# Kernel tuning notes

Measured on AMD Instinct MI355X. Metric: run time of the kernel, lower is better.

## Reference

```python
import jax, jax.numpy as jnp
import numpy as np

N = 50000          # total nodes
E = 800000         # edges (avg degree 16)
IN = 128           # in_feat
HID = 64           # hidden per head
HEADS = (4, 4, 1)
NEG_SLOPE = 0.2    # DGL GATConv leaky_relu default


def setup_inputs() -> dict:
    key = jax.random.key(0)
    ks = jax.random.split(key, 16)

    def w(k, shape, fan_in):
        return jax.random.normal(k, shape, jnp.float32) / np.float32(np.sqrt(fan_in))

    inp = {
        "feat": jax.random.normal(ks[0], (N, IN), jnp.float32),
        "src": jax.random.randint(ks[1], (E,), 0, N, jnp.int32),
        "dst": jax.random.randint(ks[2], (E,), 0, N, jnp.int32),
    }
    dims = [(IN, HEADS[0]), (HID * HEADS[0], HEADS[1]), (HID * HEADS[1], HEADS[2])]
    j = 3
    for i, (din, h) in enumerate(dims, 1):
        inp[f"W{i}"] = w(ks[j], (din, h * HID), din); j += 1
        inp[f"al{i}"] = w(ks[j], (h, HID), HID); j += 1
        inp[f"ar{i}"] = w(ks[j], (h, HID), HID); j += 1
        inp[f"b{i}"] = jnp.zeros((h * HID,), jnp.float32)
    return inp


def gat_layer(x, W, al, ar, b, src, dst, n_heads):
    # DGL GATConv: linear -> per-node attn logits -> edge leaky_relu ->
    # per-dst segment softmax -> weighted scatter-sum -> + bias
    h = (x @ W).reshape(N, n_heads, HID)                     # [N,H,D]
    el = jnp.einsum("nhd,hd->nh", h, al)                     # [N,H]
    er = jnp.einsum("nhd,hd->nh", h, ar)                     # [N,H]
    e = jax.nn.leaky_relu(el[src] + er[dst], NEG_SLOPE)      # [E,H]
    m = jax.ops.segment_max(e, dst, num_segments=N)          # [N,H]
    m = jnp.where(jnp.isfinite(m), m, 0.0)                   # empty segments -> -inf
    ex = jnp.exp(e - m[dst])                                 # [E,H]
    s = jax.ops.segment_sum(ex, dst, num_segments=N)         # [N,H]
    alpha = ex / s[dst]                                      # [E,H]
    msg = h[src] * alpha[:, :, None]                         # [E,H,D]
    out = jax.ops.segment_sum(msg, dst, num_segments=N)      # [N,H,D]
    return out + b.reshape(1, n_heads, HID)


def reference(feat, src, dst, W1, al1, ar1, b1, W2, al2, ar2, b2, W3, al3, ar3, b3):
    h = jax.nn.elu(gat_layer(feat, W1, al1, ar1, b1, src, dst, HEADS[0]))
    h = h.reshape(N, HEADS[0] * HID)                         # flatten heads
    h = jax.nn.elu(gat_layer(h, W2, al2, ar2, b2, src, dst, HEADS[1]))
    h = h.reshape(N, HEADS[1] * HID)
    h = gat_layer(h, W3, al3, ar3, b3, src, dst, HEADS[2])   # no activation
    return h.mean(axis=1)                                    # [N, HID]
```

## Files before the change

kernel.cpp:

```cpp
#include <hip/hip_runtime.h>
#include <math.h>

#define HID 64
#define NSLOPE 0.2f
#define SB 512

typedef __attribute__((ext_vector_type(8))) short short8v;
typedef __attribute__((ext_vector_type(4))) float float4v;

__device__ inline unsigned short f2bf(float x) {
  unsigned u = __float_as_uint(x);
  u += 0x7fffu + ((u >> 16) & 1u);
  return (unsigned short)(u >> 16);
}
__device__ inline float bf2f(unsigned short h) {
  return __uint_as_float(((unsigned)h) << 16);
}
__device__ inline float bflo(unsigned u) { return __uint_as_float(u << 16); }
__device__ inline float bfhi(unsigned u) { return __uint_as_float(u & 0xffff0000u); }

__global__ __launch_bounds__(256) void k_split(const float* __restrict__ x,
    unsigned short* __restrict__ hi, unsigned short* __restrict__ lo, int n) {
  int i = blockIdx.x * 256 + threadIdx.x;
  if (i < n) {
    float v = x[i];
    unsigned short h = f2bf(v);
    hi[i] = h;
    lo[i] = f2bf(v - bf2f(h));
  }
}

__global__ __launch_bounds__(256) void k_wsplit(const float* __restrict__ W,
    unsigned short* __restrict__ Whi, unsigned short* __restrict__ Wlo, int K, int N) {
  int i = blockIdx.x * 256 + threadIdx.x;
  if (i < N * K) {
    int n = i / K, k = i - n * K;
    float v = W[(size_t)k * N + n];
    unsigned short h = f2bf(v);
    Whi[i] = h;
    Wlo[i] = f2bf(v - bf2f(h));
  }
}

__global__ __launch_bounds__(256) void gemm_split(
    const unsigned short* __restrict__ Ahi, const unsigned short* __restrict__ Alo,
    const unsigned short* __restrict__ Bhi, const unsigned short* __restrict__ Blo,
    float* __restrict__ C, unsigned short* __restrict__ Gp, int M, int Nc, int K, int H) {
  __shared__ __align__(16) unsigned short AsHi[128 * 40];
  __shared__ __align__(16) unsigned short AsLo[128 * 40];
  __shared__ __align__(16) unsigned short BsHi[128 * 40];
  __shared__ __align__(16) unsigned short BsLo[128 * 40];
  const int tid = threadIdx.x;
  const int lane = tid & 63, wid = tid >> 6;
  const int wr = wid >> 1, wc = wid & 1;
  const int row0 = blockIdx.y * 128;
  const int col0 = blockIdx.x * 128;
  float4v acc[4][4];
  #pragma unroll
  for (int mi = 0; mi < 4; ++mi)
    #pragma unroll
    for (int ni = 0; ni < 4; ++ni)
      acc[mi][ni] = (float4v){0.f, 0.f, 0.f, 0.f};

  const int sr = tid >> 2;
  const int sc8 = (tid & 3) * 8;
  const int lr = lane & 15, lk = (lane >> 4) * 8;

  for (int k0 = 0; k0 < K; k0 += 32) {
    #pragma unroll
    for (int half = 0; half < 2; ++half) {
      int row = sr + half * 64;
      int arow = row0 + row; if (arow > M - 1) arow = M - 1;
      int brow = col0 + row; if (brow > Nc - 1) brow = Nc - 1;
      *(short8v*)&AsHi[row * 40 + sc8] = *(const short8v*)&Ahi[(size_t)arow * K + k0 + sc8];
      *(short8v*)&AsLo[row * 40 + sc8] = *(const short8v*)&Alo[(size_t)arow * K + k0 + sc8];
      *(short8v*)&BsHi[row * 40 + sc8] = *(const short8v*)&Bhi[(size_t)brow * K + k0 + sc8];
      *(short8v*)&BsLo[row * 40 + sc8] = *(const short8v*)&Blo[(size_t)brow * K + k0 + sc8];
    }
    __syncthreads();
    short8v ah[4], alv[4], bh[4], bl[4];
    #pragma unroll
    for (int mi = 0; mi < 4; ++mi) {
      int r = wr * 64 + mi * 16 + lr;
      ah[mi]  = *(const short8v*)&AsHi[r * 40 + lk];
      alv[mi] = *(const short8v*)&AsLo[r * 40 + lk];
    }
    #pragma unroll
    for (int ni = 0; ni < 4; ++ni) {
      int r = wc * 64 + ni * 16 + lr;
      bh[ni] = *(const short8v*)&BsHi[r * 40 + lk];
      bl[ni] = *(const short8v*)&BsLo[r * 40 + lk];
    }
    #pragma unroll
    for (int mi = 0; mi < 4; ++mi)
      #pragma unroll
      for (int ni = 0; ni < 4; ++ni) {
        acc[mi][ni] = __builtin_amdgcn_mfma_f32_16x16x32_bf16(ah[mi], bh[ni], acc[mi][ni], 0, 0, 0);
        acc[mi][ni] = __builtin_amdgcn_mfma_f32_16x16x32_bf16(ah[mi], bl[ni], acc[mi][ni], 0, 0, 0);
        acc[mi][ni] = __builtin_amdgcn_mfma_f32_16x16x32_bf16(alv[mi], bh[ni], acc[mi][ni], 0, 0, 0);
      }
    __syncthreads();
  }
  #pragma unroll
  for (int mi = 0; mi < 4; ++mi) {
    int rbase = row0 + wr * 64 + mi * 16 + (lane >> 4) * 4;
    #pragma unroll
    for (int ni = 0; ni < 4; ++ni) {
      int cc = col0 + wc * 64 + ni * 16 + (lane & 15);
      if (cc < Nc) {
        int gcol = (cc & 63) * H + (cc >> 6);
        #pragma unroll
        for (int q = 0; q < 4; ++q) {
          int rr = rbase + q;
          if (rr < M) {
            float v = acc[mi][ni][q];
            C[(size_t)rr * Nc + cc] = v;
            Gp[(size_t)rr * Nc + gcol] = f2bf(v);
          }
        }
      }
    }
  }
}

__global__ __launch_bounds__(256) void elr_kernel(const float* __restrict__ h,
    const float* __restrict__ al, const float* __restrict__ ar,
    float* __restrict__ el, float* __restrict__ er, int H, int N) {
  int n = blockIdx.x * 4 + (threadIdx.x >> 6);
  int lane = threadIdx.x & 63;
  if (n >= N) return;
  const float* hr = h + (size_t)n * H * HID;
  for (int hh = 0; hh < H; ++hh) {
    float v = hr[hh * HID + lane];
    float a = v * al[hh * HID + lane];
    float b = v * ar[hh * HID + lane];
    #pragma unroll
    for (int o = 32; o > 0; o >>= 1) { a += __shfl_xor(a, o); b += __shfl_xor(b, o); }
    if (lane == 0) { el[n * H + hh] = a; er[n * H + hh] = b; }
  }
}

__global__ void k_count(const int* __restrict__ dst, int* __restrict__ deg, int E) {
  int e = blockIdx.x * blockDim.x + threadIdx.x;
  if (e < E) atomicAdd(&deg[dst[e]], 1);
}
__global__ __launch_bounds__(SB) void k_blocksums(const int* __restrict__ deg,
                                                  int* __restrict__ bsums, int n) {
  __shared__ int s[SB];
  int t = threadIdx.x, i = blockIdx.x * SB + t;
  s[t] = (i < n) ? deg[i] : 0;
  __syncthreads();
  for (int o = SB >> 1; o > 0; o >>= 1) { if (t < o) s[t] += s[t + o]; __syncthreads(); }
  if (t == 0) bsums[blockIdx.x] = s[0];
}
__global__ __launch_bounds__(SB) void k_scancarry(const int* __restrict__ bsums,
                                                   int* __restrict__ carry, int nb) {
  __shared__ int s[SB];
  int t = threadIdx.x;
  int v = (t < nb) ? bsums[t] : 0;
  s[t] = v; __syncthreads();
  for (int o = 1; o < SB; o <<= 1) {
    int u = (t >= o) ? s[t - o] : 0;
    __syncthreads(); s[t] += u; __syncthreads();
  }
  if (t < nb) carry[t] = s[t] - v;
}
__global__ __launch_bounds__(SB) void k_offsets(const int* __restrict__ deg,
    const int* __restrict__ carry, int* __restrict__ offs, int n, int E) {
  __shared__ int s[SB];
  int t = threadIdx.x, i = blockIdx.x * SB + t;
  int v = (i < n) ? deg[i] : 0;
  s[t] = v; __syncthreads();
  for (int o = 1; o < SB; o <<= 1) {
    int u = (t >= o) ? s[t - o] : 0;
    __syncthreads(); s[t] += u; __syncthreads();
  }
  if (i < n) offs[i] = carry[blockIdx.x] + s[t] - v;
  if (i == n) offs[n] = E;
}
__global__ void k_fill(const int* __restrict__ src, const int* __restrict__ dst,
                       const int* __restrict__ offs, int* __restrict__ cursor,
                       int* __restrict__ esrc, int* __restrict__ edst, int E) {
  int e = blockIdx.x * blockDim.x + threadIdx.x;
  if (e < E) {
    int d = dst[e];
    int slot = offs[d] + atomicAdd(&cursor[d], 1);
    esrc[slot] = src[e];
    edst[slot] = d;
  }
}

template<int H>
__global__ __launch_bounds__(256) void k_exp(const float* __restrict__ el,
    const float* __restrict__ er, const int* __restrict__ esrc,
    const int* __restrict__ edst, float* __restrict__ ex, int E) {
  int e = blockIdx.x * 256 + threadIdx.x;
  if (e >= E) return;
  int s = esrc[e], d = edst[e];
  if (H == 4) {
    float4 L = *(const float4*)&el[s * 4];
    float4 R = *(const float4*)&er[d * 4];
    float4 o;
    float v;
    v = L.x + R.x; v = v > 0.f ? v : NSLOPE * v; o.x = __expf(fminf(v, 80.f));
    v = L.y + R.y; v = v > 0.f ? v : NSLOPE * v; o.y = __expf(fminf(v, 80.f));
    v = L.z + R.z; v = v > 0.f ? v : NSLOPE * v; o.z = __expf(fminf(v, 80.f));
    v = L.w + R.w; v = v > 0.f ? v : NSLOPE * v; o.w = __expf(fminf(v, 80.f));
    *(float4*)&ex[(size_t)e * 4] = o;
  } else {
    float v = el[s] + er[d];
    v = v > 0.f ? v : NSLOPE * v;
    ex[e] = __expf(fminf(v, 80.f));
  }
}

template<int H, bool DO_ELU, bool SPLITOUT>
__global__ __launch_bounds__(64) void agg_kernel(const unsigned short* __restrict__ gp,
    const float* __restrict__ ex,
    const int* __restrict__ offs, const int* __restrict__ esrc,
    const float* __restrict__ bias,
    unsigned short* __restrict__ outHi, unsigned short* __restrict__ outLo,
    float* __restrict__ outF) {
  const int n = blockIdx.x, lane = threadIdx.x;
  const int off = offs[n];
  const int deg = offs[n + 1] - off;
  float sum[H];
  #pragma unroll
  for (int h = 0; h < H; ++h) sum[h] = 0.f;
  for (int base = 0; base < deg; base += 64) {
    int i = base + lane;
    if (i < deg) {
      if (H == 4) {
        float4 x = *(const float4*)&ex[(size_t)(off + i) * 4];
        sum[0] += x.x; sum[1] += x.y; sum[2] += x.z; sum[3] += x.w;
      } else {
        sum[0] += ex[off + i];
      }
    }
  }
  float inv[H];
  #pragma unroll
  for (int h = 0; h < H; ++h) {
    float v = sum[h];
    #pragma unroll
    for (int o = 32; o > 0; o >>= 1) v += __shfl_xor(v, o);
    inv[h] = v > 0.f ? 1.f / v : 0.f;
  }
  float acc[H];
  #pragma unroll
  for (int h = 0; h < H; ++h) acc[h] = 0.f;
  int t = 0;
  for (; t + 4 <= deg; t += 4) {
    int s0 = esrc[off + t + 0], s1 = esrc[off + t + 1];
    int s2 = esrc[off + t + 2], s3 = esrc[off + t + 3];
    if (H == 4) {
      float4 x0 = *(const float4*)&ex[(size_t)(off + t + 0) * 4];
      float4 x1 = *(const float4*)&ex[(size_t)(off + t + 1) * 4];
      float4 x2 = *(const float4*)&ex[(size_t)(off + t + 2) * 4];
      float4 x3 = *(const float4*)&ex[(size_t)(off + t + 3) * 4];
      uint2 g0 = *(const uint2*)&gp[(size_t)s0 * 256 + lane * 4];
      uint2 g1 = *(const uint2*)&gp[(size_t)s1 * 256 + lane * 4];
      uint2 g2 = *(const uint2*)&gp[(size_t)s2 * 256 + lane * 4];
      uint2 g3 = *(const uint2*)&gp[(size_t)s3 * 256 + lane * 4];
      acc[0] = fmaf(bflo(g0.x), x0.x, acc[0]);
      acc[1] = fmaf(bfhi(g0.x), x0.y, acc[1]);
      acc[2] = fmaf(bflo(g0.y), x0.z, acc[2]);
      acc[3] = fmaf(bfhi(g0.y), x0.w, acc[3]);
      acc[0] = fmaf(bflo(g1.x), x1.x, acc[0]);
      acc[1] = fmaf(bfhi(g1.x), x1.y, acc[1]);
      acc[2] = fmaf(bflo(g1.y), x1.z, acc[2]);
      acc[3] = fmaf(bfhi(g1.y), x1.w, acc[3]);
      acc[0] = fmaf(bflo(g2.x), x2.x, acc[0]);
      acc[1] = fmaf(bfhi(g2.x), x2.y, acc[1]);
      acc[2] = fmaf(bflo(g2.y), x2.z, acc[2]);
      acc[3] = fmaf(bfhi(g2.y), x2.w, acc[3]);
      acc[0] = fmaf(bflo(g3.x), x3.x, acc[0]);
      acc[1] = fmaf(bfhi(g3.x), x3.y, acc[1]);
      acc[2] = fmaf(bflo(g3.y), x3.z, acc[2]);
      acc[3] = fmaf(bfhi(g3.y), x3.w, acc[3]);
    } else {
      float x0 = ex[off + t + 0], x1 = ex[off + t + 1];
      float x2 = ex[off + t + 2], x3 = ex[off + t + 3];
      float g0 = bf2f(gp[(size_t)s0 * 64 + lane]);
      float g1 = bf2f(gp[(size_t)s1 * 64 + lane]);
      float g2 = bf2f(gp[(size_t)s2 * 64 + lane]);
      float g3 = bf2f(gp[(size_t)s3 * 64 + lane]);
      acc[0] = fmaf(g0, x0, acc[0]);
      acc[0] = fmaf(g1, x1, acc[0]);
      acc[0] = fmaf(g2, x2, acc[0]);
      acc[0] = fmaf(g3, x3, acc[0]);
    }
  }
  for (; t < deg; ++t) {
    int s = esrc[off + t];
    if (H == 4) {
      float4 x = *(const float4*)&ex[(size_t)(off + t) * 4];
      uint2 g = *(const uint2*)&gp[(size_t)s * 256 + lane * 4];
      acc[0] = fmaf(bflo(g.x), x.x, acc[0]);
      acc[1] = fmaf(bfhi(g.x), x.y, acc[1]);
      acc[2] = fmaf(bflo(g.y), x.z, acc[2]);
      acc[3] = fmaf(bfhi(g.y), x.w, acc[3]);
    } else {
      acc[0] = fmaf(bf2f(gp[(size_t)s * 64 + lane]), ex[off + t], acc[0]);
    }
  }
  #pragma unroll
  for (int hh = 0; hh < H; ++hh) {
    float v = fmaf(acc[hh], inv[hh], bias[hh * HID + lane]);
    if (DO_ELU) v = v > 0.f ? v : expm1f(v);
    size_t oi = (size_t)n * (H * HID) + hh * HID + lane;
    if (SPLITOUT) {
      unsigned short hb = f2bf(v);
      outHi[oi] = hb;
      outLo[oi] = f2bf(v - bf2f(hb));
    } else {
      outF[oi] = v;
    }
  }
}

extern "C" void kernel_launch(void* const* d_in, const int* in_sizes, int n_in,
                              void* d_out, int out_size, void* d_ws, size_t ws_size,
                              hipStream_t stream) {
  const float* feat = (const float*)d_in[0];
  const int* src = (const int*)d_in[1];
  const int* dst = (const int*)d_in[2];
  const float* W1 = (const float*)d_in[3];
  const float* al1 = (const float*)d_in[4];
  const float* ar1 = (const float*)d_in[5];
  const float* b1 = (const float*)d_in[6];
  const float* W2 = (const float*)d_in[7];
  const float* al2 = (const float*)d_in[8];
  const float* ar2 = (const float*)d_in[9];
  const float* b2 = (const float*)d_in[10];
  const float* W3 = (const float*)d_in[11];
  const float* al3 = (const float*)d_in[12];
  const float* ar3 = (const float*)d_in[13];
  const float* b3 = (const float*)d_in[14];
  const int N = in_sizes[0] / 128;
  const int E = in_sizes[1];

  char* w = (char*)d_ws;
  auto alloc = [&](size_t bytes) {
    void* p = (void*)w;
    w += (bytes + 255) & ~(size_t)255;
    return p;
  };
  unsigned short* pHi = (unsigned short*)alloc((size_t)N * 256 * 2);
  unsigned short* pLo = (unsigned short*)alloc((size_t)N * 256 * 2);
  float* Cbuf = (float*)alloc((size_t)N * 256 * 4);
  unsigned short* Gp = (unsigned short*)alloc((size_t)N * 256 * 2);
  float* el = (float*)alloc((size_t)N * 4 * 4);
  float* er = (float*)alloc((size_t)N * 4 * 4);
  float* exbuf = (float*)alloc((size_t)E * 4 * 4);
  int* deg = (int*)alloc((size_t)N * 4);
  int* cursor = (int*)alloc((size_t)N * 4);
  int* offs = (int*)alloc((size_t)(N + 1) * 4);
  int nb = (N + SB - 1) / SB;
  int* bsums = (int*)alloc((size_t)nb * 4);
  int* carry = (int*)alloc((size_t)nb * 4);
  int* esrc = (int*)alloc((size_t)E * 4);
  int* edst = (int*)alloc((size_t)E * 4);
  unsigned short* W1h = (unsigned short*)alloc((size_t)256 * 128 * 2);
  unsigned short* W1l = (unsigned short*)alloc((size_t)256 * 128 * 2);
  unsigned short* W2h = (unsigned short*)alloc((size_t)256 * 256 * 2);
  unsigned short* W2l = (unsigned short*)alloc((size_t)256 * 256 * 2);
  unsigned short* W3h = (unsigned short*)alloc((size_t)64 * 256 * 2);
  unsigned short* W3l = (unsigned short*)alloc((size_t)64 * 256 * 2);

  hipMemsetAsync(deg, 0, (size_t)N * 4, stream);
  hipMemsetAsync(cursor, 0, (size_t)N * 4, stream);
  int eb = (E + 255) / 256;
  k_count<<<eb, 256, 0, stream>>>(dst, deg, E);
  k_blocksums<<<nb, SB, 0, stream>>>(deg, bsums, N);
  k_scancarry<<<1, SB, 0, stream>>>(bsums, carry, nb);
  k_offsets<<<nb, SB, 0, stream>>>(deg, carry, offs, N, E);
  k_fill<<<eb, 256, 0, stream>>>(src, dst, offs, cursor, esrc, edst, E);

  k_wsplit<<<(256 * 128 + 255) / 256, 256, 0, stream>>>(W1, W1h, W1l, 128, 256);
  k_wsplit<<<(256 * 256 + 255) / 256, 256, 0, stream>>>(W2, W2h, W2l, 256, 256);
  k_wsplit<<<(64 * 256 + 255) / 256, 256, 0, stream>>>(W3, W3h, W3l, 256, 64);

  k_split<<<((N * 128) + 255) / 256, 256, 0, stream>>>(feat, pHi, pLo, N * 128);

  int rg = (N + 127) / 128;
  int ng4 = (N + 3) / 4;
  gemm_split<<<dim3(2, rg), 256, 0, stream>>>(pHi, pLo, W1h, W1l, Cbuf, Gp, N, 256, 128, 4);
  elr_kernel<<<ng4, 256, 0, stream>>>(Cbuf, al1, ar1, el, er, 4, N);
  k_exp<4><<<eb, 256, 0, stream>>>(el, er, esrc, edst, exbuf, E);
  agg_kernel<4, true, true><<<N, 64, 0, stream>>>(Gp, exbuf, offs, esrc, b1, pHi, pLo, nullptr);
  gemm_split<<<dim3(2, rg), 256, 0, stream>>>(pHi, pLo, W2h, W2l, Cbuf, Gp, N, 256, 256, 4);
  elr_kernel<<<ng4, 256, 0, stream>>>(Cbuf, al2, ar2, el, er, 4, N);
  k_exp<4><<<eb, 256, 0, stream>>>(el, er, esrc, edst, exbuf, E);
  agg_kernel<4, true, true><<<N, 64, 0, stream>>>(Gp, exbuf, offs, esrc, b2, pHi, pLo, nullptr);
  gemm_split<<<dim3(1, rg), 256, 0, stream>>>(pHi, pLo, W3h, W3l, Cbuf, Gp, N, 64, 256, 1);
  elr_kernel<<<ng4, 256, 0, stream>>>(Cbuf, al3, ar3, el, er, 1, N);
  k_exp<1><<<eb, 256, 0, stream>>>(el, er, esrc, edst, exbuf, E);
  agg_kernel<1, false, false><<<N, 64, 0, stream>>>(Gp, exbuf, offs, esrc, b3, nullptr, nullptr, (float*)d_out);
}
```

Before: 481.2 us.

## Fuse edge exp computation into aggregation kernel with LDS staging

Removes the separate k_exp kernel and its E*H exbuf round trip. Each aggregation block now computes the leaky-relu exp logits for its incoming edges, keeps up to EXCAP values in shared memory for the weighted gather, and recomputes them for any edges beyond the cap. This also drops the edst array from k_fill. The cost is extra el gathers inside the agg kernel and 8KB of LDS per 64-thread block, which may lower occupancy.

```diff
diff --git a/kernel.cpp b/kernel.cpp
--- a/kernel.cpp
+++ b/kernel.cpp
@@ -4,6 +4,7 @@
 #define HID 64
 #define NSLOPE 0.2f
 #define SB 512
+#define EXCAP 512
 
 typedef __attribute__((ext_vector_type(8))) short short8v;
 typedef __attribute__((ext_vector_type(4))) float float4v;
@@ -180,61 +181,59 @@
 }
 __global__ void k_fill(const int* __restrict__ src, const int* __restrict__ dst,
                        const int* __restrict__ offs, int* __restrict__ cursor,
-                       int* __restrict__ esrc, int* __restrict__ edst, int E) {
+                       int* __restrict__ esrc, int E) {
   int e = blockIdx.x * blockDim.x + threadIdx.x;
   if (e < E) {
     int d = dst[e];
     int slot = offs[d] + atomicAdd(&cursor[d], 1);
     esrc[slot] = src[e];
-    edst[slot] = d;
-  }
-}
-
-template<int H>
-__global__ __launch_bounds__(256) void k_exp(const float* __restrict__ el,
-    const float* __restrict__ er, const int* __restrict__ esrc,
-    const int* __restrict__ edst, float* __restrict__ ex, int E) {
-  int e = blockIdx.x * 256 + threadIdx.x;
-  if (e >= E) return;
-  int s = esrc[e], d = edst[e];
-  if (H == 4) {
-    float4 L = *(const float4*)&el[s * 4];
-    float4 R = *(const float4*)&er[d * 4];
-    float4 o;
-    float v;
-    v = L.x + R.x; v = v > 0.f ? v : NSLOPE * v; o.x = __expf(fminf(v, 80.f));
-    v = L.y + R.y; v = v > 0.f ? v : NSLOPE * v; o.y = __expf(fminf(v, 80.f));
-    v = L.z + R.z; v = v > 0.f ? v : NSLOPE * v; o.z = __expf(fminf(v, 80.f));
-    v = L.w + R.w; v = v > 0.f ? v : NSLOPE * v; o.w = __expf(fminf(v, 80.f));
-    *(float4*)&ex[(size_t)e * 4] = o;
-  } else {
-    float v = el[s] + er[d];
-    v = v > 0.f ? v : NSLOPE * v;
-    ex[e] = __expf(fminf(v, 80.f));
   }
 }
 
 template<int H, bool DO_ELU, bool SPLITOUT>
 __global__ __launch_bounds__(64) void agg_kernel(const unsigned short* __restrict__ gp,
-    const float* __restrict__ ex,
+    const float* __restrict__ el, const float* __restrict__ er,
     const int* __restrict__ offs, const int* __restrict__ esrc,
     const float* __restrict__ bias,
     unsigned short* __restrict__ outHi, unsigned short* __restrict__ outLo,
     float* __restrict__ outF) {
+  __shared__ __align__(16) float exs[EXCAP * H];
   const int n = blockIdx.x, lane = threadIdx.x;
   const int off = offs[n];
   const int deg = offs[n + 1] - off;
+  float ern[H];
+  if (H == 4) {
+    float4 R = *(const float4*)&er[n * 4];
+    ern[0] = R.x; ern[1] = R.y; ern[2] = R.z; ern[3] = R.w;
+  } else {
+    ern[0] = er[n];
+  }
   float sum[H];
   #pragma unroll
   for (int h = 0; h < H; ++h) sum[h] = 0.f;
   for (int base = 0; base < deg; base += 64) {
     int i = base + lane;
     if (i < deg) {
+      int s = esrc[off + i];
       if (H == 4) {
-        float4 x = *(const float4*)&ex[(size_t)(off + i) * 4];
-        sum[0] += x.x; sum[1] += x.y; sum[2] += x.z; sum[3] += x.w;
+        float4 L = *(const float4*)&el[s * 4];
+        float lv[4] = {L.x, L.y, L.z, L.w};
+        float exv[4];
+        #pragma unroll
+        for (int h = 0; h < 4; ++h) {
+          float e = lv[h] + ern[h];
+          e = e > 0.f ? e : NSLOPE * e;
+          exv[h] = __expf(fminf(e, 80.f));
+          sum[h] += exv[h];
+        }
+        if (i < EXCAP)
+          *(float4*)&exs[i * 4] = make_float4(exv[0], exv[1], exv[2], exv[3]);
       } else {
-        sum[0] += ex[off + i];
+        float e = el[s] + ern[0];
+        e = e > 0.f ? e : NSLOPE * e;
+        float x = __expf(fminf(e, 80.f));
+        sum[0] += x;
+        if (i < EXCAP) exs[i] = x;
       }
     }
   }
@@ -246,18 +245,20 @@
     for (int o = 32; o > 0; o >>= 1) v += __shfl_xor(v, o);
     inv[h] = v > 0.f ? 1.f / v : 0.f;
   }
+  __syncthreads();
   float acc[H];
   #pragma unroll
   for (int h = 0; h < H; ++h) acc[h] = 0.f;
+  const int degc = deg < EXCAP ? deg : EXCAP;
   int t = 0;
-  for (; t + 4 <= deg; t += 4) {
+  for (; t + 4 <= degc; t += 4) {
     int s0 = esrc[off + t + 0], s1 = esrc[off + t + 1];
     int s2 = esrc[off + t + 2], s3 = esrc[off + t + 3];
     if (H == 4) {
-      float4 x0 = *(const float4*)&ex[(size_t)(off + t + 0) * 4];
-      float4 x1 = *(const float4*)&ex[(size_t)(off + t + 1) * 4];
-      float4 x2 = *(const float4*)&ex[(size_t)(off + t + 2) * 4];
-      float4 x3 = *(const float4*)&ex[(size_t)(off + t + 3) * 4];
+      float4 x0 = *(const float4*)&exs[(t + 0) * 4];
+      float4 x1 = *(const float4*)&exs[(t + 1) * 4];
+      float4 x2 = *(const float4*)&exs[(t + 2) * 4];
+      float4 x3 = *(const float4*)&exs[(t + 3) * 4];
       uint2 g0 = *(const uint2*)&gp[(size_t)s0 * 256 + lane * 4];
       uint2 g1 = *(const uint2*)&gp[(size_t)s1 * 256 + lane * 4];
       uint2 g2 = *(const uint2*)&gp[(size_t)s2 * 256 + lane * 4];
@@ -279,8 +280,7 @@
       acc[2] = fmaf(bflo(g3.y), x3.z, acc[2]);
       acc[3] = fmaf(bfhi(g3.y), x3.w, acc[3]);
     } else {
-      float x0 = ex[off + t + 0], x1 = ex[off + t + 1];
-      float x2 = ex[off + t + 2], x3 = ex[off + t + 3];
+      float x0 = exs[t + 0], x1 = exs[t + 1], x2 = exs[t + 2], x3 = exs[t + 3];
       float g0 = bf2f(gp[(size_t)s0 * 64 + lane]);
       float g1 = bf2f(gp[(size_t)s1 * 64 + lane]);
       float g2 = bf2f(gp[(size_t)s2 * 64 + lane]);
@@ -291,17 +291,29 @@
       acc[0] = fmaf(g3, x3, acc[0]);
     }
   }
-  for (; t < deg; ++t) {
+  for (; t < degc; ++t) {
     int s = esrc[off + t];
     if (H == 4) {
-      float4 x = *(const float4*)&ex[(size_t)(off + t) * 4];
+      float4 x = *(const float4*)&exs[t * 4];
       uint2 g = *(const uint2*)&gp[(size_t)s * 256 + lane * 4];
       acc[0] = fmaf(bflo(g.x), x.x, acc[0]);
       acc[1] = fmaf(bfhi(g.x), x.y, acc[1]);
       acc[2] = fmaf(bflo(g.y), x.z, acc[2]);
       acc[3] = fmaf(bfhi(g.y), x.w, acc[3]);
     } else {
-      acc[0] = fmaf(bf2f(gp[(size_t)s * 64 + lane]), ex[off + t], acc[0]);
+      acc[0] = fmaf(bf2f(gp[(size_t)s * 64 + lane]), exs[t], acc[0]);
+    }
+  }
+  for (; t < deg; ++t) {
+    int s = esrc[off + t];
+    #pragma unroll
+    for (int hh = 0; hh < H; ++hh) {
+      float e = el[s * H + hh] + ern[hh];
+      e = e > 0.f ? e : NSLOPE * e;
+      float x = __expf(fminf(e, 80.f));
+      float v = (H == 4) ? bf2f(gp[(size_t)s * 256 + lane * 4 + hh])
+                         : bf2f(gp[(size_t)s * 64 + lane]);
+      acc[hh] = fmaf(v, x, acc[hh]);
     }
   }
   #pragma unroll
@@ -352,7 +364,6 @@
   unsigned short* Gp = (unsigned short*)alloc((size_t)N * 256 * 2);
   float* el = (float*)alloc((size_t)N * 4 * 4);
   float* er = (float*)alloc((size_t)N * 4 * 4);
-  float* exbuf = (float*)alloc((size_t)E * 4 * 4);
   int* deg = (int*)alloc((size_t)N * 4);
   int* cursor = (int*)alloc((size_t)N * 4);
   int* offs = (int*)alloc((size_t)(N + 1) * 4);
@@ -360,7 +371,6 @@
   int* bsums = (int*)alloc((size_t)nb * 4);
   int* carry = (int*)alloc((size_t)nb * 4);
   int* esrc = (int*)alloc((size_t)E * 4);
-  int* edst = (int*)alloc((size_t)E * 4);
   unsigned short* W1h = (unsigned short*)alloc((size_t)256 * 128 * 2);
   unsigned short* W1l = (unsigned short*)alloc((size_t)256 * 128 * 2);
   unsigned short* W2h = (unsigned short*)alloc((size_t)256 * 256 * 2);
@@ -375,7 +385,7 @@
   k_blocksums<<<nb, SB, 0, stream>>>(deg, bsums, N);
   k_scancarry<<<1, SB, 0, stream>>>(bsums, carry, nb);
   k_offsets<<<nb, SB, 0, stream>>>(deg, carry, offs, N, E);
-  k_fill<<<eb, 256, 0, stream>>>(src, dst, offs, cursor, esrc, edst, E);
+  k_fill<<<eb, 256, 0, stream>>>(src, dst, offs, cursor, esrc, E);
 
   k_wsplit<<<(256 * 128 + 255) / 256, 256, 0, stream>>>(W1, W1h, W1l, 128, 256);
   k_wsplit<<<(256 * 256 + 255) / 256, 256, 0, stream>>>(W2, W2h, W2l, 256, 256);
@@ -387,14 +397,11 @@
   int ng4 = (N + 3) / 4;
   gemm_split<<<dim3(2, rg), 256, 0, stream>>>(pHi, pLo, W1h, W1l, Cbuf, Gp, N, 256, 128, 4);
   elr_kernel<<<ng4, 256, 0, stream>>>(Cbuf, al1, ar1, el, er, 4, N);
-  k_exp<4><<<eb, 256, 0, stream>>>(el, er, esrc, edst, exbuf, E);
-  agg_kernel<4, true, true><<<N, 64, 0, stream>>>(Gp, exbuf, offs, esrc, b1, pHi, pLo, nullptr);
+  agg_kernel<4, true, true><<<N, 64, 0, stream>>>(Gp, el, er, offs, esrc, b1, pHi, pLo, nullptr);
   gemm_split<<<dim3(2, rg), 256, 0, stream>>>(pHi, pLo, W2h, W2l, Cbuf, Gp, N, 256, 256, 4);
   elr_kernel<<<ng4, 256, 0, stream>>>(Cbuf, al2, ar2, el, er, 4, N);
-  k_exp<4><<<eb, 256, 0, stream>>>(el, er, esrc, edst, exbuf, E);
-  agg_kernel<4, true, true><<<N, 64, 0, stream>>>(Gp, exbuf, offs, esrc, b2, pHi, pLo, nullptr);
+  agg_kernel<4, true, true><<<N, 64, 0, stream>>>(Gp, el, er, offs, esrc, b2, pHi, pLo, nullptr);
   gemm_split<<<dim3(1, rg), 256, 0, stream>>>(pHi, pLo, W3h, W3l, Cbuf, Gp, N, 64, 256, 1);
   elr_kernel<<<ng4, 256, 0, stream>>>(Cbuf, al3, ar3, el, er, 1, N);
-  k_exp<1><<<eb, 256, 0, stream>>>(el, er, esrc, edst, exbuf, E);
-  agg_kernel<1, false, false><<<N, 64, 0, stream>>>(Gp, exbuf, offs, esrc, b3, nullptr, nullptr, (float*)d_out);
-}
+  agg_kernel<1, false, false><<<N, 64, 0, stream>>>(Gp, el, er, offs, esrc, b3, nullptr, nullptr, (float*)d_out);
+}
```

Measured after the change: 464.4 us. 1.04x faster.
